# Optimization experiments

Measured on AMD Instinct MI355X. Metric: run time of the kernel, lower is better.

## Reference

```python
import jax, jax.numpy as jnp
import numpy as np

B, N, T, F = 16, 512, 24, 64


def setup_inputs() -> dict:
    key = jax.random.key(0)
    k1, k2, k3, k4 = jax.random.split(key, 4)
    ori_flow = jax.random.normal(k1, (B, N, T, F), dtype=jnp.float32)
    uncer = jax.random.normal(k2, (B, N, T, F), dtype=jnp.float32)
    spatial_embedding = jax.random.normal(k3, (N, F), dtype=jnp.float32)
    # nn.Linear(channels, channels, bias=False): y = x @ W.T, W: (out, in)
    W1 = jax.random.normal(k4, (F, F), dtype=jnp.float32) * (1.0 / np.sqrt(F))
    return {"ori_flow": ori_flow, "uncer": uncer,
            "spatial_embedding": spatial_embedding, "W1": W1}


def reference(ori_flow, uncer, spatial_embedding, W1):
    b, n, t, f = ori_flow.shape
    # (B, N, T, f) -> (B*T, N, f)
    x = ori_flow.transpose(0, 2, 1, 3).reshape(-1, n, f)
    u = uncer.transpose(0, 2, 1, 3).reshape(-1, n, f)
    # spatial embedding is identical across batch and time after expand/permute
    emb = jnp.broadcast_to(spatial_embedding, (b * t, n, f))
    h = jnp.concatenate([x, emb], axis=-1)            # (B*T, N, 2f)
    rel = jax.nn.relu(jnp.einsum('bnf,bmf->bnm', h, h))  # (B*T, N, N)
    rel = jax.nn.softmax(rel, axis=-1)                # dropout p=0 -> identity
    # sharing_paras=True: both branches use linear1 (no bias)
    of = jax.nn.relu(jnp.einsum('bnm,bmf->bnf', rel, x) @ W1.T)
    uf = jax.nn.relu(jnp.einsum('bnm,bmf->bnf', rel, u) @ W1.T)
    of = of.reshape(b, t, n, f).transpose(0, 2, 1, 3)  # (B, N, T, f)
    uf = uf.reshape(b, t, n, f).transpose(0, 2, 1, 3)
    return of, uf
```

## Files before the change

### kernel.cpp

```cpp
#include <hip/hip_runtime.h>
#include <hip/hip_bf16.h>

#define BB 16
#define NN 512
#define TT 24
#define FF 64
#define OUT_OFF ((size_t)BB*NN*TT*FF)

#define AIS 136
#define XTS 72
#define XTSZ 4672

typedef __attribute__((ext_vector_type(8))) short v8s;
typedef __attribute__((ext_vector_type(16))) float v16f;

union U16x8 { uint4 v; unsigned int u[4]; unsigned short s[8]; };

__device__ inline v16f mfma32(v8s a, v8s b, v16f c) {
    return __builtin_amdgcn_mfma_f32_32x32x16_bf16(a, b, c, 0, 0, 0);
}

__device__ inline unsigned int fbits(float x) {
    union { float f; unsigned int u; } c; c.f = x; return c.u;
}
__device__ inline float ibits(unsigned int u) {
    union { float f; unsigned int u; } c; c.u = u; return c.f;
}
__device__ inline unsigned short f2bf_r(float x) {
    return (unsigned short)((fbits(x) + 0x8000u) >> 16);
}
__device__ inline unsigned int pkbf(float a, float b) {
    unsigned int r;
    asm("v_cvt_pk_bf16_f32 %0, %1, %2" : "=v"(r) : "v"(a), "v"(b));
    return r;
}
__device__ inline void split8(const float* f, U16x8& H, U16x8& L) {
    #pragma unroll
    for (int k = 0; k < 4; ++k) {
        unsigned int hp = pkbf(f[2*k], f[2*k+1]);
        float h0 = ibits(hp << 16);
        float h1 = ibits(hp & 0xffff0000u);
        L.u[k] = pkbf(f[2*k] - h0, f[2*k+1] - h1);
        H.u[k] = hp;
    }
}
__device__ inline void cvt8h(const float* f, U16x8& H) {
    #pragma unroll
    for (int k = 0; k < 8; ++k) H.s[k] = f2bf_r(f[k]);
}

__device__ inline v8s pfrag(const float* cr, int c) {
    unsigned int a0 = pkbf(cr[8*c+0], cr[8*c+1]);
    unsigned int a1 = pkbf(cr[8*c+2], cr[8*c+3]);
    unsigned int b0 = pkbf(cr[8*c+4], cr[8*c+5]);
    unsigned int b1 = pkbf(cr[8*c+6], cr[8*c+7]);
    asm("v_permlane32_swap_b32 %0, %1" : "+v"(a0), "+v"(b0));
    asm("v_permlane32_swap_b32 %0, %1" : "+v"(a1), "+v"(b1));
    union { v8s v; unsigned int u[4]; } P;
    P.u[0] = a0; P.u[1] = a1; P.u[2] = b0; P.u[3] = b1;
    return P.v;
}

__global__ __launch_bounds__(256, 2)
void spag_kernel(const float* __restrict__ ori, const float* __restrict__ unc,
                 const float* __restrict__ emb, const float* __restrict__ W1,
                 float* __restrict__ out)
{
    __shared__ __align__(16) unsigned short SH[2*64*AIS + 2*XTSZ];
    unsigned short* AjH = SH;
    unsigned short* AjL = SH + 64*AIS;
    unsigned short* XT  = SH + 2*64*AIS;
    unsigned short* UT  = XT + XTSZ;

    const int tid  = threadIdx.x;
    const int xcd  = blockIdx.x & 7;
    const int slot = blockIdx.x >> 3;
    const int bt   = xcd * 48 + (slot >> 2);
    const int it   = slot & 3;
    const int b    = bt / TT, t = bt % TT;
    const int i0   = it * 128;

    const int lane = tid & 63;
    const int w    = tid >> 6;
    const int m    = lane & 31;
    const int hi   = lane >> 5;

    const int pj  = tid >> 3;
    const int f0  = (tid & 7) * 8;
    const int jme = 2 * pj;

    float pa0[8], pa1[8], pu0[8], pu1[8];
    {
        const size_t r0 = ((size_t)((b*NN + jme)*TT + t))*FF + f0;
        const size_t r1 = r0 + (size_t)TT*FF;
        *(float4*)&pa0[0] = *(const float4*)(ori + r0);
        *(float4*)&pa0[4] = *(const float4*)(ori + r0 + 4);
        *(float4*)&pa1[0] = *(const float4*)(ori + r1);
        *(float4*)&pa1[4] = *(const float4*)(ori + r1 + 4);
        *(float4*)&pu0[0] = *(const float4*)(unc + r0);
        *(float4*)&pu0[4] = *(const float4*)(unc + r0 + 4);
        *(float4*)&pu1[0] = *(const float4*)(unc + r1);
        *(float4*)&pu1[4] = *(const float4*)(unc + r1 + 4);
    }

    v8s bH[8], bL[8];
    #pragma unroll
    for (int p = 0; p < 2; ++p) {
        {
            const int sr = tid >> 2, fc = (tid & 3) * 16;
            const float* xb = ori + ((size_t)((b*NN + i0 + p*64 + sr)*TT + t))*FF + fc;
            const float* eb = emb + (size_t)(i0 + p*64 + sr)*FF + fc;
            float tf[8]; U16x8 H, L;
            #pragma unroll
            for (int h = 0; h < 2; ++h) {
                *(float4*)&tf[0] = ((const float4*)xb)[2*h];
                *(float4*)&tf[4] = ((const float4*)xb)[2*h+1];
                split8(tf, H, L);
                *(uint4*)&AjH[sr*AIS + fc + h*8] = H.v;
                *(uint4*)&AjL[sr*AIS + fc + h*8] = L.v;
                *(float4*)&tf[0] = ((const float4*)eb)[2*h];
                *(float4*)&tf[4] = ((const float4*)eb)[2*h+1];
                split8(tf, H, L);
                *(uint4*)&AjH[sr*AIS + 64 + fc + h*8] = H.v;
                *(uint4*)&AjL[sr*AIS + 64 + fc + h*8] = L.v;
            }
        }
        __syncthreads();
        if ((w >> 1) == p) {
            const int lr = (w & 1)*32 + m;
            #pragma unroll
            for (int kk = 0; kk < 8; ++kk) {
                bH[kk] = *(const v8s*)&AjH[lr*AIS + kk*16 + hi*8];
                bL[kk] = *(const v8s*)&AjL[lr*AIS + kk*16 + hi*8];
            }
        }
        __syncthreads();
    }

    v16f accX0 = (v16f)(0.0f), accX1 = (v16f)(0.0f);
    v16f accU0 = (v16f)(0.0f), accU1 = (v16f)(0.0f);
    float rs    = 0.0f;
    float m_run = 0.0f;

    for (int jt = 0; jt < 8; ++jt) {
        const int j0 = jt * 64;
        __syncthreads();

        {
            const int j = jme;
            U16x8 H0, L0, H1, L1;
            split8(pa0, H0, L0); split8(pa1, H1, L1);
            *(uint4*)&AjH[ j   *AIS + f0] = H0.v;
            *(uint4*)&AjH[(j+1)*AIS + f0] = H1.v;
            *(uint4*)&AjL[ j   *AIS + f0] = L0.v;
            *(uint4*)&AjL[(j+1)*AIS + f0] = L1.v;
            #pragma unroll
            for (int k = 0; k < 8; ++k) {
                int f = f0 + k;
                int off = f*XTS + (f>>4)*16 + j;
                *(unsigned int*)&XT[off] = pkbf(pa0[k], pa1[k]);
                *(unsigned int*)&UT[off] = pkbf(pu0[k], pu1[k]);
            }
            const float* e0 = emb + (size_t)(j0 + j)*FF + f0;
            float t0[8], t1[8];
            *(float4*)&t0[0] = *(const float4*)(e0);
            *(float4*)&t0[4] = *(const float4*)(e0 + 4);
            *(float4*)&t1[0] = *(const float4*)(e0 + FF);
            *(float4*)&t1[4] = *(const float4*)(e0 + FF + 4);
            split8(t0, H0, L0); split8(t1, H1, L1);
            *(uint4*)&AjH[ j   *AIS + 64 + f0] = H0.v;
            *(uint4*)&AjH[(j+1)*AIS + 64 + f0] = H1.v;
            *(uint4*)&AjL[ j   *AIS + 64 + f0] = L0.v;
            *(uint4*)&AjL[(j+1)*AIS + 64 + f0] = L1.v;
        }
        __syncthreads();

        if (jt < 7) {
            const size_t r0 = ((size_t)((b*NN + j0 + 64 + jme)*TT + t))*FF + f0;
            const size_t r1 = r0 + (size_t)TT*FF;
            *(float4*)&pa0[0] = *(const float4*)(ori + r0);
            *(float4*)&pa0[4] = *(const float4*)(ori + r0 + 4);
            *(float4*)&pa1[0] = *(const float4*)(ori + r1);
            *(float4*)&pa1[4] = *(const float4*)(ori + r1 + 4);
            *(float4*)&pu0[0] = *(const float4*)(unc + r0);
            *(float4*)&pu0[4] = *(const float4*)(unc + r0 + 4);
            *(float4*)&pu1[0] = *(const float4*)(unc + r1);
            *(float4*)&pu1[4] = *(const float4*)(unc + r1 + 4);
        }

        __builtin_amdgcn_s_setprio(1);
        v16f C0 = (v16f)(0.0f), C1 = (v16f)(0.0f);
        #pragma unroll
        for (int kk = 0; kk < 8; ++kk) {
            const int fo = kk*16 + hi*8;
            v8s aH0 = *(const v8s*)&AjH[ m     *AIS + fo];
            v8s aL0 = *(const v8s*)&AjL[ m     *AIS + fo];
            v8s aH1 = *(const v8s*)&AjH[(32+m)*AIS + fo];
            v8s aL1 = *(const v8s*)&AjL[(32+m)*AIS + fo];
            C0 = mfma32(aH0, bH[kk], C0);
            C1 = mfma32(aH1, bH[kk], C1);
            C0 = mfma32(aH0, bL[kk], C0);
            C1 = mfma32(aH1, bL[kk], C1);
            C0 = mfma32(aL0, bH[kk], C0);
            C1 = mfma32(aL1, bH[kk], C1);
        }
        __builtin_amdgcn_s_setprio(0);

        float mt = 0.0f;
        #pragma unroll
        for (int r = 0; r < 16; ++r) {
            float s0 = fmaxf(C0[r], 0.0f); C0[r] = s0;
            float s1 = fmaxf(C1[r], 0.0f); C1[r] = s1;
            mt = fmaxf(mt, fmaxf(s0, s1));
        }
        mt = fmaxf(mt, __shfl_xor(mt, 32));
        if (!__all(mt <= m_run + 8.0f)) {
            float m_new = fmaxf(m_run, mt);
            float al = __expf(m_run - m_new);
            rs *= al; m_run = m_new;
            #pragma unroll
            for (int r = 0; r < 16; ++r) {
                float a = __shfl(al, (r & 3) + 8*(r >> 2) + 4*hi);
                accX0[r] *= a; accX1[r] *= a;
                accU0[r] *= a; accU1[r] *= a;
            }
        }

        v8s P[4];
        {
            float cr[16];
            #pragma unroll
            for (int r = 0; r < 16; ++r) {
                float e = __expf(C0[r] - m_run);
                cr[r] = e;
                rs += e;
            }
            P[0] = pfrag(cr, 0);
            P[1] = pfrag(cr, 1);
            #pragma unroll
            for (int r = 0; r < 16; ++r) {
                float e = __expf(C1[r] - m_run);
                cr[r] = e;
                rs += e;
            }
            P[2] = pfrag(cr, 0);
            P[3] = pfrag(cr, 1);
        }

        __builtin_amdgcn_s_setprio(1);
        #pragma unroll
        for (int kk = 0; kk < 4; ++kk) {
            const int fo = kk*16 + hi*8;
            v8s bx0 = *(const v8s*)&XT[ m     *XTS + (( m    )>>4)*16 + fo];
            v8s bu0 = *(const v8s*)&UT[ m     *XTS + (( m    )>>4)*16 + fo];
            v8s bx1 = *(const v8s*)&XT[(32+m)*XTS + (((32+m))>>4)*16 + fo];
            v8s bu1 = *(const v8s*)&UT[(32+m)*XTS + (((32+m))>>4)*16 + fo];
            accX0 = mfma32(P[kk], bx0, accX0);
            accX1 = mfma32(P[kk], bx1, accX1);
            accU0 = mfma32(P[kk], bu0, accU0);
            accU1 = mfma32(P[kk], bu1, accU1);
        }
        __builtin_amdgcn_s_setprio(0);
    }

    __syncthreads();
    rs += __shfl_xor(rs, 32);
    float inv = 1.0f / rs;

    unsigned short* Ox = SH;
    unsigned short* Ou = SH + 128*XTS;
    unsigned short* Wt = SH + 256*XTS;

    #pragma unroll
    for (int r = 0; r < 16; ++r) {
        int il = (r & 3) + 8*(r >> 2) + 4*hi;
        float iv = __shfl(inv, il);
        int row = w*32 + il;
        Ox[row*XTS + m]      = f2bf_r(accX0[r] * iv);
        Ox[row*XTS + 32 + m] = f2bf_r(accX1[r] * iv);
        Ou[row*XTS + m]      = f2bf_r(accU0[r] * iv);
        Ou[row*XTS + 32 + m] = f2bf_r(accU1[r] * iv);
    }
    {
        const int sr = tid >> 2, fc = (tid & 3) * 16;
        const float* wb = W1 + sr*FF + fc;
        float tf[8]; U16x8 H;
        #pragma unroll
        for (int h = 0; h < 2; ++h) {
            *(float4*)&tf[0] = ((const float4*)wb)[2*h];
            *(float4*)&tf[4] = ((const float4*)wb)[2*h+1];
            cvt8h(tf, H);
            *(uint4*)&Wt[sr*XTS + fc + h*8] = H.v;
        }
    }
    __syncthreads();

    v8s ao[4], aq[4];
    #pragma unroll
    for (int kk = 0; kk < 4; ++kk) {
        const int fo = kk*16 + hi*8;
        ao[kk] = *(const v8s*)&Ox[(w*32 + m)*XTS + fo];
        aq[kk] = *(const v8s*)&Ou[(w*32 + m)*XTS + fo];
    }
    #pragma unroll
    for (int ot = 0; ot < 2; ++ot) {
        v16f ax = (v16f)(0.0f), au = (v16f)(0.0f);
        #pragma unroll
        for (int kk = 0; kk < 4; ++kk) {
            const int fo = kk*16 + hi*8;
            v8s bw = *(const v8s*)&Wt[(ot*32 + m)*XTS + fo];
            ax = mfma32(ao[kk], bw, ax);
            au = mfma32(aq[kk], bw, au);
        }
        #pragma unroll
        for (int r = 0; r < 16; ++r) {
            int il = (r & 3) + 8*(r >> 2) + 4*hi;
            int i = i0 + w*32 + il;
            int o = ot*32 + m;
            size_t idx = ((size_t)((b*NN + i)*TT + t))*FF + o;
            out[idx]           = fmaxf(ax[r], 0.0f);
            out[OUT_OFF + idx] = fmaxf(au[r], 0.0f);
        }
    }
}

extern "C" void kernel_launch(void* const* d_in, const int* in_sizes, int n_in,
                              void* d_out, int out_size, void* d_ws, size_t ws_size,
                              hipStream_t stream) {
    const float* ori = (const float*)d_in[0];
    const float* unc = (const float*)d_in[1];
    const float* emb = (const float*)d_in[2];
    const float* W1  = (const float*)d_in[3];
    float* out = (float*)d_out;

    spag_kernel<<<dim3(BB*TT*4), dim3(256), 0, stream>>>(ori, unc, emb, W1, out);
}
```

Before: 256.9 us.

## Split QK^T tile staging to overlap first-half MFMA with embedding and transpose stores

```diff
diff --git a/kernel.cpp b/kernel.cpp
--- a/kernel.cpp
+++ b/kernel.cpp
@@ -146,32 +146,52 @@
         const int j0 = jt * 64;
         __syncthreads();
 
+        float t0[8], t1[8];
         {
-            const int j = jme;
-            U16x8 H0, L0, H1, L1;
-            split8(pa0, H0, L0); split8(pa1, H1, L1);
-            *(uint4*)&AjH[ j   *AIS + f0] = H0.v;
-            *(uint4*)&AjH[(j+1)*AIS + f0] = H1.v;
-            *(uint4*)&AjL[ j   *AIS + f0] = L0.v;
-            *(uint4*)&AjL[(j+1)*AIS + f0] = L1.v;
-            #pragma unroll
-            for (int k = 0; k < 8; ++k) {
-                int f = f0 + k;
-                int off = f*XTS + (f>>4)*16 + j;
-                *(unsigned int*)&XT[off] = pkbf(pa0[k], pa1[k]);
-                *(unsigned int*)&UT[off] = pkbf(pu0[k], pu1[k]);
-            }
-            const float* e0 = emb + (size_t)(j0 + j)*FF + f0;
-            float t0[8], t1[8];
+            const float* e0 = emb + (size_t)(j0 + jme)*FF + f0;
             *(float4*)&t0[0] = *(const float4*)(e0);
             *(float4*)&t0[4] = *(const float4*)(e0 + 4);
             *(float4*)&t1[0] = *(const float4*)(e0 + FF);
             *(float4*)&t1[4] = *(const float4*)(e0 + FF + 4);
+
+            U16x8 H0, L0, H1, L1;
+            split8(pa0, H0, L0); split8(pa1, H1, L1);
+            *(uint4*)&AjH[ jme   *AIS + f0] = H0.v;
+            *(uint4*)&AjH[(jme+1)*AIS + f0] = H1.v;
+            *(uint4*)&AjL[ jme   *AIS + f0] = L0.v;
+            *(uint4*)&AjL[(jme+1)*AIS + f0] = L1.v;
+        }
+        __syncthreads();
+
+        {
+            U16x8 H0, L0, H1, L1;
             split8(t0, H0, L0); split8(t1, H1, L1);
-            *(uint4*)&AjH[ j   *AIS + 64 + f0] = H0.v;
-            *(uint4*)&AjH[(j+1)*AIS + 64 + f0] = H1.v;
-            *(uint4*)&AjL[ j   *AIS + 64 + f0] = L0.v;
-            *(uint4*)&AjL[(j+1)*AIS + 64 + f0] = L1.v;
+            *(uint4*)&AjH[ jme   *AIS + 64 + f0] = H0.v;
+            *(uint4*)&AjH[(jme+1)*AIS + 64 + f0] = H1.v;
+            *(uint4*)&AjL[ jme   *AIS + 64 + f0] = L0.v;
+            *(uint4*)&AjL[(jme+1)*AIS + 64 + f0] = L1.v;
+            #pragma unroll
+            for (int k = 0; k < 8; ++k) {
+                int f = f0 + k;
+                int off = f*XTS + (f>>4)*16 + jme;
+                *(unsigned int*)&XT[off] = pkbf(pa0[k], pa1[k]);
+                *(unsigned int*)&UT[off] = pkbf(pu0[k], pu1[k]);
+            }
+        }
+        v16f C0 = (v16f)(0.0f), C1 = (v16f)(0.0f);
+        #pragma unroll
+        for (int kk = 0; kk < 4; ++kk) {
+            const int fo = kk*16 + hi*8;
+            v8s aH0 = *(const v8s*)&AjH[ m     *AIS + fo];
+            v8s aL0 = *(const v8s*)&AjL[ m     *AIS + fo];
+            v8s aH1 = *(const v8s*)&AjH[(32+m)*AIS + fo];
+            v8s aL1 = *(const v8s*)&AjL[(32+m)*AIS + fo];
+            C0 = mfma32(aH0, bH[kk], C0);
+            C1 = mfma32(aH1, bH[kk], C1);
+            C0 = mfma32(aH0, bL[kk], C0);
+            C1 = mfma32(aH1, bL[kk], C1);
+            C0 = mfma32(aL0, bH[kk], C0);
+            C1 = mfma32(aL1, bH[kk], C1);
         }
         __syncthreads();
 
@@ -188,10 +208,8 @@
             *(float4*)&pu1[4] = *(const float4*)(unc + r1 + 4);
         }
 
-        __builtin_amdgcn_s_setprio(1);
-        v16f C0 = (v16f)(0.0f), C1 = (v16f)(0.0f);
-        #pragma unroll
-        for (int kk = 0; kk < 8; ++kk) {
+        #pragma unroll
+        for (int kk = 4; kk < 8; ++kk) {
             const int fo = kk*16 + hi*8;
             v8s aH0 = *(const v8s*)&AjH[ m     *AIS + fo];
             v8s aL0 = *(const v8s*)&AjL[ m     *AIS + fo];
@@ -204,7 +222,6 @@
             C0 = mfma32(aL0, bH[kk], C0);
             C1 = mfma32(aL1, bH[kk], C1);
         }
-        __builtin_amdgcn_s_setprio(0);
 
         float mt = 0.0f;
         #pragma unroll
@@ -247,7 +264,6 @@
             P[3] = pfrag(cr, 1);
         }
 
-        __builtin_amdgcn_s_setprio(1);
         #pragma unroll
         for (int kk = 0; kk < 4; ++kk) {
             const int fo = kk*16 + hi*8;
@@ -260,7 +276,6 @@
             accU0 = mfma32(P[kk], bu0, accU0);
             accU1 = mfma32(P[kk], bu1, accU1);
         }
-        __builtin_amdgcn_s_setprio(0);
     }
 
     __syncthreads();
```

Result: no change. 255.3 us (-0.6%).
